# Performance work log

Measured on AMD Instinct MI355X. Metric: run time of the kernel, lower is better.

## Reference

```python
import jax, jax.numpy as jnp
import numpy as np

SOS = 1

def setup_inputs() -> dict:
    key = jax.random.key(0)
    ks = jax.random.split(key, 12)
    B, S, T, H, V = 64, 128, 32, 1024, 32000
    sc = 0.02
    return {
        'encoder_outputs': jax.random.normal(ks[0], (B, S, H), jnp.float32),
        'encoder_hidden': jax.random.normal(ks[1], (1, B, H), jnp.float32),
        'target_tensor': jax.random.randint(ks[2], (B, T), 0, V),
        'embedding': jax.random.normal(ks[3], (V, H), jnp.float32) * sc,
        'Wa': jax.random.normal(ks[4], (H, H), jnp.float32) * sc,
        'ba': jnp.zeros((H,), jnp.float32),
        'Ua': jax.random.normal(ks[5], (H, H), jnp.float32) * sc,
        'bu': jnp.zeros((H,), jnp.float32),
        'Va': jax.random.normal(ks[6], (1, H), jnp.float32) * sc,
        'bv': jnp.zeros((1,), jnp.float32),
        'W_ih': jax.random.normal(ks[7], (3 * H, 2 * H), jnp.float32) * sc,
        'b_ih': jnp.zeros((3 * H,), jnp.float32),
        'W_hh': jax.random.normal(ks[8], (3 * H, H), jnp.float32) * sc,
        'b_hh': jnp.zeros((3 * H,), jnp.float32),
        'W_out': jax.random.normal(ks[9], (V, H), jnp.float32) * sc,
        'b_out': jnp.zeros((V,), jnp.float32),
    }

def reference(encoder_outputs, encoder_hidden, target_tensor, embedding,
              Wa, ba, Ua, bu, Va, bv, W_ih, b_ih, W_hh, b_hh, W_out, b_out):
    B, S, H = encoder_outputs.shape
    T = target_tensor.shape[1]
    # teacher forcing: input at step i is SOS for i=0 else target[:, i-1]
    tokens = jnp.concatenate([jnp.full((B, 1), SOS, target_tensor.dtype),
                              target_tensor[:, :-1]], axis=1)  # (B,T)
    emb = embedding[tokens]  # (B,T,H); dropout is identity (eval)
    keys_proj = jnp.einsum('bsh,gh->bsg', encoder_outputs, Ua) + bu  # Ua(keys), (B,S,H)
    h0 = encoder_hidden[0]  # (B,H)

    def step(h, x_t):
        # Bahdanau attention: Va(tanh(Wa q + Ua k))
        q = h @ Wa.T + ba  # (B,H)
        scores = jnp.einsum('bsh,h->bs', jnp.tanh(q[:, None, :] + keys_proj), Va[0]) + bv[0]
        w = jax.nn.softmax(scores, axis=-1)  # (B,S)
        ctx = jnp.einsum('bs,bsh->bh', w, encoder_outputs)
        x = jnp.concatenate([x_t, ctx], axis=-1)  # (B,2H)
        # GRU cell (PyTorch convention)
        gi = x @ W_ih.T + b_ih
        gh = h @ W_hh.T + b_hh
        ir, iz, inn = jnp.split(gi, 3, axis=-1)
        hr, hz, hn = jnp.split(gh, 3, axis=-1)
        r = jax.nn.sigmoid(ir + hr)
        z = jax.nn.sigmoid(iz + hz)
        n = jnp.tanh(inn + r * hn)
        h_new = (1.0 - z) * n + z * h
        logits = h_new @ W_out.T + b_out  # (B,V)
        return h_new, (logits, w)

    h_final, (logits, weights) = jax.lax.scan(step, h0, jnp.swapaxes(emb, 0, 1))
    log_probs = jax.nn.log_softmax(jnp.swapaxes(logits, 0, 1), axis=-1)  # (B,T,V)
    attentions = jnp.swapaxes(weights, 0, 1)  # (B,T,S)
    return log_probs, h_final[None], attentions
```

## Files before the change

### kernel.cpp

```cpp
#include <hip/hip_runtime.h>


typedef unsigned short u16;
typedef __bf16 bf16x8 __attribute__((ext_vector_type(8)));
typedef float f32x4 __attribute__((ext_vector_type(4)));
typedef u16 u16x8 __attribute__((ext_vector_type(8)));

#define DEV __device__ __forceinline__

DEV u16 f2b(float f) {
  union { float f; unsigned u; } v; v.f = f;
  unsigned r = v.u + 0x7fffu + ((v.u >> 16) & 1u);
  return (u16)(r >> 16);
}
DEV float b2f(u16 b) {
  union { unsigned u; float f; } v; v.u = ((unsigned)b) << 16;
  return v.f;
}
DEV float sigm(float x) { return 1.f / (1.f + __expf(-x)); }
DEV float ftanh(float x) {
  x = fminf(fmaxf(x, -20.f), 20.f);
  float e = __expf(2.f * x);
  return (e - 1.f) / (e + 1.f);
}
DEV void gl16(const void* g, void* l) {
  __builtin_amdgcn_global_load_lds((const __attribute__((address_space(1))) void*)g,
                                   (__attribute__((address_space(3))) void*)l, 16, 0, 0);
}

__global__ __launch_bounds__(256) void prepk(const float* __restrict__ enc, const float* __restrict__ Ua,
                                             const float* __restrict__ Wa, const float* __restrict__ Whh,
                                             const float* __restrict__ Wout, const float* __restrict__ Wih,
                                             const float* __restrict__ embd, const int* __restrict__ tgt,
                                             const float* __restrict__ eh, u16* __restrict__ enc_b,
                                             u16* __restrict__ Ua_b, u16* __restrict__ Wa_b,
                                             u16* __restrict__ Whh_b, u16* __restrict__ Wout_b,
                                             u16* __restrict__ Wih1_b, u16* __restrict__ Wih2_b,
                                             u16* __restrict__ emb_b, float* __restrict__ hf,
                                             u16* __restrict__ hb0) {
  const long q0 = 2097152;
  const long q1 = q0 + 262144;
  const long q2 = q1 + 262144;
  const long q3 = q2 + 786432;
  const long q4 = q3 + 8192000;
  const long q5 = q4 + 1572864;
  const long q6 = q5 + 524288;
  const long q7 = q6 + 16384;
  long stride = (long)gridDim.x * 256;
  for (long i = (long)blockIdx.x * 256 + threadIdx.x; i < q7; i += stride) {
    if (i < q4) {
      const float* src; u16* dst; long off;
      if (i < q0) { src = enc; dst = enc_b; off = i; }
      else if (i < q1) { src = Ua; dst = Ua_b; off = i - q0; }
      else if (i < q2) { src = Wa; dst = Wa_b; off = i - q1; }
      else if (i < q3) { src = Whh; dst = Whh_b; off = i - q2; }
      else { src = Wout; dst = Wout_b; off = i - q3; }
      float4 v = ((const float4*)src)[off];
      ushort4 o; o.x = f2b(v.x); o.y = f2b(v.y); o.z = f2b(v.z); o.w = f2b(v.w);
      ((ushort4*)dst)[off] = o;
    } else if (i < q5) {
      long off = i - q4;
      long e = off * 4;
      int row = (int)(e >> 11), col = (int)(e & 2047);
      float4 v = ((const float4*)Wih)[off];
      ushort4 o; o.x = f2b(v.x); o.y = f2b(v.y); o.z = f2b(v.z); o.w = f2b(v.w);
      u16* dst = (col < 1024) ? (Wih1_b + (size_t)row * 1024 + col)
                              : (Wih2_b + (size_t)row * 1024 + col - 1024);
      *(ushort4*)dst = o;
    } else if (i < q6) {
      long off = i - q5;
      size_t e = (size_t)off * 4;
      int h = (int)(e & 1023);
      int bt = (int)(e >> 10);
      int b = bt >> 5, t = bt & 31;
      int tok = (t == 0) ? 1 : tgt[b * 32 + t - 1];
      const float* src = embd + (size_t)tok * 1024 + h;
      float4 v = *(const float4*)src;
      ushort4 o; o.x = f2b(v.x); o.y = f2b(v.y); o.z = f2b(v.z); o.w = f2b(v.w);
      *(ushort4*)(emb_b + e) = o;
    } else {
      long off = i - q6;
      float4 v = ((const float4*)eh)[off];
      ((float4*)hf)[off] = v;
      ushort4 o; o.x = f2b(v.x); o.y = f2b(v.y); o.z = f2b(v.z); o.w = f2b(v.w);
      ((ushort4*)hb0)[off] = o;
    }
  }
}

template <int MODE>
__global__ __launch_bounds__(256) void gemm_tile(const u16* __restrict__ A, const u16* __restrict__ Bm,
                                                 const float* __restrict__ bias, float* __restrict__ Cf,
                                                 u16* __restrict__ Cb, int K, int ldc, int nTM) {
  __shared__ __attribute__((aligned(16))) u16 As[128 * 32];
  __shared__ __attribute__((aligned(16))) u16 Bs[128 * 32];
  const int tid = threadIdx.x, lane = tid & 63, w = tid >> 6;
  const int chunk = gridDim.x >> 3, wg = blockIdx.x;
  const int id = (wg & 7) * chunk + (wg >> 3);
  const int m = id % nTM, n = id / nTM;
  const int m0 = m * 128, n0 = n * 128;
  const int wm = w >> 1, wn = w & 1;
  const int l16 = lane & 15, kg = lane >> 4;
  const int srow = lane >> 2;
  const int skk = (((lane & 3) ^ ((srow >> 1) & 3)) * 8);
  const int slot = (kg ^ ((l16 >> 1) & 3)) * 8;

  f32x4 acc[4][4];
#pragma unroll
  for (int i = 0; i < 4; ++i)
#pragma unroll
    for (int j = 0; j < 4; ++j) acc[i][j] = f32x4{0.f, 0.f, 0.f, 0.f};

  for (int k0 = 0; k0 < K; k0 += 32) {
#pragma unroll
    for (int ch = 0; ch < 2; ++ch) {
      int c = w + ch * 4;
      gl16(A + (size_t)(m0 + c * 16 + srow) * K + k0 + skk, &As[c * 512]);
      gl16(Bm + (size_t)(n0 + c * 16 + srow) * K + k0 + skk, &Bs[c * 512]);
    }
    __syncthreads();
    bf16x8 av[4], bv[4];
#pragma unroll
    for (int i = 0; i < 4; ++i) av[i] = *(const bf16x8*)&As[(wm * 4 + i) * 512 + l16 * 32 + slot];
#pragma unroll
    for (int j = 0; j < 4; ++j) bv[j] = *(const bf16x8*)&Bs[(wn * 4 + j) * 512 + l16 * 32 + slot];
#pragma unroll
    for (int i = 0; i < 4; ++i)
#pragma unroll
      for (int j = 0; j < 4; ++j)
        acc[i][j] = __builtin_amdgcn_mfma_f32_16x16x32_bf16(av[i], bv[j], acc[i][j], 0, 0, 0);
    __syncthreads();
  }
#pragma unroll
  for (int i = 0; i < 4; ++i) {
    int rowb = m0 + (wm * 4 + i) * 16 + kg * 4;
#pragma unroll
    for (int j = 0; j < 4; ++j) {
      int col = n0 + (wn * 4 + j) * 16 + l16;
      float bb = (MODE == 2) ? 0.f : bias[col];
#pragma unroll
      for (int r = 0; r < 4; ++r) {
        int row = rowb + r;
        float v = acc[i][j][r] + bb;
        if (MODE == 0) Cf[(size_t)row * ldc + col] = v;
        else Cb[(size_t)row * ldc + col] = f2b(v);
      }
    }
  }
}

template <int MODE, int MAP>
__global__ __launch_bounds__(256, 2) void gemm_wide(const u16* __restrict__ A, const u16* __restrict__ Bm,
                                                    const float* __restrict__ bias, float* __restrict__ Cf,
                                                    u16* __restrict__ Cb, int K, int ldc, int nTM) {
  __shared__ __attribute__((aligned(16))) u16 As[128 * 64];
  __shared__ __attribute__((aligned(16))) u16 Bs[256 * 64];
  const int tid = threadIdx.x, lane = tid & 63, w = tid >> 6;
  const int chunk = gridDim.x >> 3, wg = blockIdx.x;
  const int id = (wg & 7) * chunk + (wg >> 3);
  int m, n;
  if (MAP == 0) { int r_ = id % 80; m = r_ & 15; n = 5 * (id / 80) + (r_ >> 4); }
  else { m = id % nTM; n = id / nTM; }
  const int m0 = m * 128, n0 = n * 256;
  const int wm = w >> 1, wn = w & 1;
  const int l16 = lane & 15, kg = lane >> 4;
  const int srow = lane >> 2;
  const int skk = (((lane & 3) ^ ((srow >> 1) & 3)) * 8);
  const int slot = (kg ^ ((l16 >> 1) & 3)) * 8;

  f32x4 acc[4][8];
#pragma unroll
  for (int i = 0; i < 4; ++i)
#pragma unroll
    for (int j = 0; j < 8; ++j) acc[i][j] = f32x4{0.f, 0.f, 0.f, 0.f};

  for (int k0 = 0; k0 < K; k0 += 64) {
#pragma unroll
    for (int ch = 0; ch < 2; ++ch) {
      int c = w + ch * 4;
#pragma unroll
      for (int p = 0; p < 2; ++p)
        gl16(A + (size_t)(m0 + c * 16 + srow) * K + k0 + p * 32 + skk, &As[c * 1024 + p * 512]);
    }
#pragma unroll
    for (int ch = 0; ch < 4; ++ch) {
      int c = w + ch * 4;
#pragma unroll
      for (int p = 0; p < 2; ++p)
        gl16(Bm + (size_t)(n0 + c * 16 + srow) * K + k0 + p * 32 + skk, &Bs[c * 1024 + p * 512]);
    }
    __syncthreads();
#pragma unroll
    for (int p = 0; p < 2; ++p) {
      bf16x8 av[4], bv[8];
#pragma unroll
      for (int i = 0; i < 4; ++i)
        av[i] = *(const bf16x8*)&As[(wm * 4 + i) * 1024 + p * 512 + l16 * 32 + slot];
#pragma unroll
      for (int j = 0; j < 8; ++j)
        bv[j] = *(const bf16x8*)&Bs[(wn * 8 + j) * 1024 + p * 512 + l16 * 32 + slot];
#pragma unroll
      for (int i = 0; i < 4; ++i)
#pragma unroll
        for (int j = 0; j < 8; ++j)
          acc[i][j] = __builtin_amdgcn_mfma_f32_16x16x32_bf16(av[i], bv[j], acc[i][j], 0, 0, 0);
    }
    __syncthreads();
  }
#pragma unroll
  for (int i = 0; i < 4; ++i) {
    int rowb = m0 + (wm * 4 + i) * 16 + kg * 4;
#pragma unroll
    for (int j = 0; j < 8; ++j) {
      int col = n0 + (wn * 8 + j) * 16 + l16;
      float bb = (MODE == 2) ? 0.f : bias[col];
#pragma unroll
      for (int r = 0; r < 4; ++r) {
        int row = rowb + r;
        float v = acc[i][j][r] + bb;
        if (MODE == 2) {
          Cb[(size_t)row * ldc + col] = f2b(v);
        } else {
          int b_ = row & 63, t_ = row >> 6;
          size_t ro = ((size_t)b_ * 32 + t_) * ldc + col;
          if (MODE == 0) Cf[ro] = v; else Cb[ro] = f2b(v);
        }
      }
    }
  }
}

__global__ __launch_bounds__(256) void qkghk(const u16* __restrict__ hb, const u16* __restrict__ W1,
                                             float* __restrict__ qghp) {
  const int tid = threadIdx.x, lane = tid & 63, w = tid >> 6;
  const int l16 = lane & 15, kg = lane >> 4;
  const int pg = blockIdx.x >> 2, ks = blockIdx.x & 3;
  const u16* ap = hb + (size_t)(w * 16 + l16) * 1024 + ks * 256 + kg * 8;
  const u16* bp = W1 + (size_t)(pg * 16 + l16) * 1024 + ks * 256 + kg * 8;
  f32x4 a = {0.f, 0.f, 0.f, 0.f};
#pragma unroll
  for (int k0 = 0; k0 < 256; k0 += 32)
    a = __builtin_amdgcn_mfma_f32_16x16x32_bf16(*(const bf16x8*)(ap + k0), *(const bf16x8*)(bp + k0),
                                                a, 0, 0, 0);
  const int col = pg * 16 + l16;
#pragma unroll
  for (int r = 0; r < 4; ++r) {
    int b = w * 16 + kg * 4 + r;
    qghp[(size_t)ks * 262144 + b * 4096 + col] = a[r];
  }
}

__global__ __launch_bounds__(256) void scorekq(const float* __restrict__ qghp, const float* __restrict__ ba,
                                               const float* __restrict__ Va, const u16* __restrict__ kp,
                                               float* __restrict__ sc) {
  const int b = blockIdx.x >> 4, s16 = blockIdx.x & 15;
  const int tid = threadIdx.x, lane = tid & 63, w = tid >> 6;
  __shared__ float qs[1024], vas[1024];
#pragma unroll
  for (int j = 0; j < 4; ++j) {
    int e = tid + j * 256;
    qs[e] = qghp[b * 4096 + e] + qghp[262144 + b * 4096 + e] + qghp[524288 + b * 4096 + e] +
            qghp[786432 + b * 4096 + e] + ba[e];
    vas[e] = Va[e];
  }
  __syncthreads();
#pragma unroll
  for (int si = 0; si < 2; ++si) {
    int s = s16 * 8 + w * 2 + si;
    const bf16x8* kv = (const bf16x8*)(kp + ((size_t)b * 128 + s) * 1024);
    float a = 0.f;
#pragma unroll
    for (int i2 = 0; i2 < 2; ++i2) {
      int e = lane + 64 * i2;
      bf16x8 k8 = kv[e];
#pragma unroll
      for (int j = 0; j < 8; ++j) a += vas[e * 8 + j] * ftanh(qs[e * 8 + j] + (float)k8[j]);
    }
#pragma unroll
    for (int off = 32; off; off >>= 1) a += __shfl_xor(a, off);
    if (lane == 0) sc[b * 128 + s] = a;
  }
}

__global__ __launch_bounds__(512, 4) void wsumgate(const float* __restrict__ scb, const u16* __restrict__ encW2,
                                                   const float* __restrict__ gie, const float* __restrict__ qghp,
                                                   const float* __restrict__ bhh, float* __restrict__ hf,
                                                   u16* __restrict__ hbW, u16* __restrict__ hall,
                                                   float* __restrict__ hfin, float* __restrict__ att_out, int t) {
  const int b = blockIdx.x >> 3, ce = blockIdx.x & 7;
  const int tid = threadIdx.x, lane = tid & 63, w = tid >> 6;
  __shared__ float wsm[128];
  __shared__ float pa[32][3][128];
  if (w == 0) {
    float v0 = scb[b * 128 + lane], v1 = scb[b * 128 + 64 + lane];
    float mx = fmaxf(v0, v1);
#pragma unroll
    for (int off = 32; off; off >>= 1) mx = fmaxf(mx, __shfl_xor(mx, off));
    float e0 = __expf(v0 - mx), e1 = __expf(v1 - mx);
    float sm = e0 + e1;
#pragma unroll
    for (int off = 32; off; off >>= 1) sm += __shfl_xor(sm, off);
    float inv = 1.f / sm;
    e0 *= inv; e1 *= inv;
    wsm[lane] = e0; wsm[lane + 64] = e1;
    if (ce == 0) {
      size_t ao = ((size_t)b * 32 + t) * 128;
      att_out[ao + lane] = e0;
      att_out[ao + lane + 64] = e1;
    }
  }
  __syncthreads();
  const int cg8 = tid & 15, sg = tid >> 4;
  const int colBase = ce * 128 + cg8 * 8;
  float a0[8], a1[8], a2[8];
#pragma unroll
  for (int k = 0; k < 8; ++k) { a0[k] = 0.f; a1[k] = 0.f; a2[k] = 0.f; }
  const u16* ep = encW2 + ((size_t)b * 128 + sg * 4) * 3072 + colBase;
#pragma unroll
  for (int si = 0; si < 4; ++si) {
    float ws = wsm[sg * 4 + si];
    u16x8 v0 = *(const u16x8*)(ep);
    u16x8 v1 = *(const u16x8*)(ep + 1024);
    u16x8 v2 = *(const u16x8*)(ep + 2048);
#pragma unroll
    for (int k = 0; k < 8; ++k) {
      a0[k] += ws * b2f(v0[k]);
      a1[k] += ws * b2f(v1[k]);
      a2[k] += ws * b2f(v2[k]);
    }
    ep += 3072;
  }
  {
    f32x4 t0 = {a0[0], a0[1], a0[2], a0[3]}, t1 = {a0[4], a0[5], a0[6], a0[7]};
    *(f32x4*)&pa[sg][0][cg8 * 8] = t0; *(f32x4*)&pa[sg][0][cg8 * 8 + 4] = t1;
    f32x4 t2 = {a1[0], a1[1], a1[2], a1[3]}, t3 = {a1[4], a1[5], a1[6], a1[7]};
    *(f32x4*)&pa[sg][1][cg8 * 8] = t2; *(f32x4*)&pa[sg][1][cg8 * 8 + 4] = t3;
    f32x4 t4 = {a2[0], a2[1], a2[2], a2[3]}, t5 = {a2[4], a2[5], a2[6], a2[7]};
    *(f32x4*)&pa[sg][2][cg8 * 8] = t4; *(f32x4*)&pa[sg][2][cg8 * 8 + 4] = t5;
  }
  __syncthreads();
  if (tid < 128) {
    float g0 = 0.f, g1 = 0.f, g2 = 0.f;
#pragma unroll
    for (int s2 = 0; s2 < 32; ++s2) {
      g0 += pa[s2][0][tid]; g1 += pa[s2][1][tid]; g2 += pa[s2][2][tid];
    }
    const int c2 = ce * 128 + tid;
    const float* ge = gie + ((size_t)b * 32 + t) * 3072 + c2;
    const float* qg = qghp + (size_t)b * 4096 + 1024 + c2;
    float hr = qg[0] + qg[262144] + qg[524288] + qg[786432] + bhh[c2];
    float hz = qg[1024] + qg[1024 + 262144] + qg[1024 + 524288] + qg[1024 + 786432] + bhh[c2 + 1024];
    float hn = qg[2048] + qg[2048 + 262144] + qg[2048 + 524288] + qg[2048 + 786432] + bhh[c2 + 2048];
    float rr = sigm(g0 + ge[0] + hr);
    float zz = sigm(g1 + ge[1024] + hz);
    float nn = ftanh(g2 + ge[2048] + rr * hn);
    const int i = b * 1024 + c2;
    float hp = hf[i];
    float hv = (1.f - zz) * nn + zz * hp;
    hf[i] = hv;
    u16 h16 = f2b(hv);
    hbW[i] = h16;
    hall[((size_t)t * 64 + b) * 1024 + c2] = h16;
    if (t == 31) hfin[i] = hv;
  }
}

__global__ __launch_bounds__(256) void smaxctxk(const float* __restrict__ sc, const u16* __restrict__ encb,
                                                u16* __restrict__ ctxb, float* __restrict__ att_out, int t) {
  const int b = blockIdx.x >> 2, hq = blockIdx.x & 3;
  const int tid = threadIdx.x, lane = tid & 63, w = tid >> 6;
  __shared__ float wsm[128];
  if (w == 0) {
    float v0 = sc[b * 128 + lane], v1 = sc[b * 128 + 64 + lane];
    float mx = fmaxf(v0, v1);
#pragma unroll
    for (int off = 32; off; off >>= 1) mx = fmaxf(mx, __shfl_xor(mx, off));
    float e0 = __expf(v0 - mx), e1 = __expf(v1 - mx);
    float sm = e0 + e1;
#pragma unroll
    for (int off = 32; off; off >>= 1) sm += __shfl_xor(sm, off);
    float inv = 1.f / sm;
    e0 *= inv; e1 *= inv;
    wsm[lane] = e0; wsm[lane + 64] = e1;
    if (hq == 0) {
      size_t ao = ((size_t)b * 32 + t) * 128;
      att_out[ao + lane] = e0;
      att_out[ao + lane + 64] = e1;
    }
  }
  __syncthreads();
  const int h = hq * 256 + tid;
  const u16* ep = encb + (size_t)b * 131072 + h;
  float c = 0.f;
#pragma unroll 8
  for (int s = 0; s < 128; ++s) c += wsm[s] * b2f(ep[(size_t)s * 1024]);
  ctxb[(size_t)b * 1024 + h] = f2b(c);
}

__global__ __launch_bounds__(256) void gi2w(const u16* __restrict__ ctxb, const u16* __restrict__ Wih2,
                                            float* __restrict__ gic) {
  const int tid = threadIdx.x, lane = tid & 63, w = tid >> 6;
  const int l16 = lane & 15, kg = lane >> 4;
  const int c0 = blockIdx.x * 16;
  const u16* ap = ctxb + (size_t)(w * 16 + l16) * 1024 + kg * 8;
  const u16* bp = Wih2 + (size_t)(c0 + l16) * 1024 + kg * 8;
  f32x4 a0 = {0.f, 0.f, 0.f, 0.f}, a1 = {0.f, 0.f, 0.f, 0.f};
#pragma unroll 4
  for (int k0 = 0; k0 < 1024; k0 += 64) {
    a0 = __builtin_amdgcn_mfma_f32_16x16x32_bf16(*(const bf16x8*)(ap + k0), *(const bf16x8*)(bp + k0),
                                                 a0, 0, 0, 0);
    a1 = __builtin_amdgcn_mfma_f32_16x16x32_bf16(*(const bf16x8*)(ap + k0 + 32),
                                                 *(const bf16x8*)(bp + k0 + 32), a1, 0, 0, 0);
  }
  const int col = c0 + l16;
#pragma unroll
  for (int r = 0; r < 4; ++r) {
    int b = w * 16 + kg * 4 + r;
    gic[(size_t)b * 3072 + col] = a0[r] + a1[r];
  }
}

__global__ __launch_bounds__(256) void gatesq(const float* __restrict__ gic, const float* __restrict__ gie,
                                              const float* __restrict__ qghp, const float* __restrict__ bhh,
                                              float* __restrict__ hf, u16* __restrict__ hbW,
                                              u16* __restrict__ hall, float* __restrict__ hfin, int t) {
  const int i = blockIdx.x * 256 + threadIdx.x;
  const int b = i >> 10, col = i & 1023;
  const float* gi = gic + (size_t)b * 3072 + col;
  const float* ge = gie + ((size_t)b * 32 + t) * 3072 + col;
  const float* qg = qghp + (size_t)b * 4096 + 1024 + col;
  float hr = qg[0] + qg[262144] + qg[524288] + qg[786432] + bhh[col];
  float hz = qg[1024] + qg[1024 + 262144] + qg[1024 + 524288] + qg[1024 + 786432] + bhh[col + 1024];
  float hn = qg[2048] + qg[2048 + 262144] + qg[2048 + 524288] + qg[2048 + 786432] + bhh[col + 2048];
  float rr = sigm(gi[0] + ge[0] + hr);
  float zz = sigm(gi[1024] + ge[1024] + hz);
  float nn = ftanh(gi[2048] + ge[2048] + rr * hn);
  float hp = hf[i];
  float hv = (1.f - zz) * nn + zz * hp;
  hf[i] = hv;
  u16 h16 = f2b(hv);
  hbW[i] = h16;
  hall[((size_t)t * 64 + b) * 1024 + col] = h16;
  if (t == 31) hfin[i] = hv;
}

__global__ __launch_bounds__(256) void logsoftk(const u16* __restrict__ lg, float* __restrict__ out) {
  const int row = blockIdx.x, tid = threadIdx.x, lane = tid & 63, w = tid >> 6;
  const u16x8* p = (const u16x8*)(lg + (size_t)row * 32000);
  __shared__ float red[4];
  u16x8 d[16];
#pragma unroll
  for (int j = 0; j < 16; ++j) {
    int i = tid + j * 256;
    if (i < 4000) d[j] = p[i];
  }
  float mx = -3.0e38f;
#pragma unroll
  for (int j = 0; j < 16; ++j) {
    int i = tid + j * 256;
    if (i < 4000)
#pragma unroll
      for (int k = 0; k < 8; ++k) mx = fmaxf(mx, b2f(d[j][k]));
  }
#pragma unroll
  for (int off = 32; off; off >>= 1) mx = fmaxf(mx, __shfl_xor(mx, off));
  if (lane == 0) red[w] = mx;
  __syncthreads();
  mx = fmaxf(fmaxf(red[0], red[1]), fmaxf(red[2], red[3]));
  __syncthreads();
  float s = 0.f;
#pragma unroll
  for (int j = 0; j < 16; ++j) {
    int i = tid + j * 256;
    if (i < 4000)
#pragma unroll
      for (int k = 0; k < 8; ++k) s += __expf(b2f(d[j][k]) - mx);
  }
#pragma unroll
  for (int off = 32; off; off >>= 1) s += __shfl_xor(s, off);
  if (lane == 0) red[w] = s;
  __syncthreads();
  float c = mx + __logf(red[0] + red[1] + red[2] + red[3]);
  float* op = out + (size_t)row * 32000;
#pragma unroll
  for (int j = 0; j < 16; ++j) {
    int i = tid + j * 256;
    if (i < 4000) {
      f32x4 o0, o1;
#pragma unroll
      for (int k = 0; k < 4; ++k) { o0[k] = b2f(d[j][k]) - c; o1[k] = b2f(d[j][k + 4]) - c; }
      *(f32x4*)(op + i * 8) = o0;
      *(f32x4*)(op + i * 8 + 4) = o1;
    }
  }
}

__global__ __launch_bounds__(256) void rowstatk(const float* __restrict__ lp, float* __restrict__ c) {
  int row = blockIdx.x;
  const float4* p = (const float4*)(lp + (size_t)row * 32000);
  int tid = threadIdx.x, lane = tid & 63, w = tid >> 6;
  __shared__ float redm[4], reds[4];
  float mx = -3.0e38f;
  for (int i = tid; i < 8000; i += 256) {
    float4 v = p[i];
    mx = fmaxf(mx, fmaxf(fmaxf(v.x, v.y), fmaxf(v.z, v.w)));
  }
#pragma unroll
  for (int off = 32; off; off >>= 1) mx = fmaxf(mx, __shfl_xor(mx, off));
  if (lane == 0) redm[w] = mx;
  __syncthreads();
  mx = fmaxf(fmaxf(redm[0], redm[1]), fmaxf(redm[2], redm[3]));
  float s = 0.f;
  for (int i = tid; i < 8000; i += 256) {
    float4 v = p[i];
    s += __expf(v.x - mx) + __expf(v.y - mx) + __expf(v.z - mx) + __expf(v.w - mx);
  }
#pragma unroll
  for (int off = 32; off; off >>= 1) s += __shfl_xor(s, off);
  if (lane == 0) reds[w] = s;
  __syncthreads();
  if (tid == 0) c[row] = mx + __logf(reds[0] + reds[1] + reds[2] + reds[3]);
}

__global__ __launch_bounds__(256) void subk(float* __restrict__ lp, const float* __restrict__ c) {
  const long n4 = (long)64 * 32 * 32000 / 4;
  long stride = (long)gridDim.x * 256;
  for (long i = (long)blockIdx.x * 256 + threadIdx.x; i < n4; i += stride) {
    float4 v = ((float4*)lp)[i];
    float cc = c[i / 8000];
    v.x -= cc; v.y -= cc; v.z -= cc; v.w -= cc;
    ((float4*)lp)[i] = v;
  }
}

extern "C" void kernel_launch(void* const* d_in, const int* in_sizes, int n_in, void* d_out, int out_size,
                              void* d_ws, size_t ws_size, hipStream_t stream) {
  (void)in_sizes; (void)n_in; (void)out_size;
  constexpr int B = 64, S = 128, T = 32, H = 1024, V = 32000;

  const float* enc  = (const float*)d_in[0];
  const float* ehid = (const float*)d_in[1];
  const int*   tgt  = (const int*)d_in[2];
  const float* embd = (const float*)d_in[3];
  const float* Wa   = (const float*)d_in[4];
  const float* ba   = (const float*)d_in[5];
  const float* Ua   = (const float*)d_in[6];
  const float* bu   = (const float*)d_in[7];
  const float* Va   = (const float*)d_in[8];
  const float* Wih  = (const float*)d_in[10];
  const float* bih  = (const float*)d_in[11];
  const float* Whh  = (const float*)d_in[12];
  const float* bhh  = (const float*)d_in[13];
  const float* Wout = (const float*)d_in[14];
  const float* bout = (const float*)d_in[15];

  char* wp = (char*)d_ws;
  auto alloc = [&](size_t bytes) {
    char* p = wp;
    wp += (bytes + 255) & ~(size_t)255;
    return p;
  };
  u16* enc_b  = (u16*)alloc((size_t)B * S * H * 2);
  u16* kp_b   = (u16*)alloc((size_t)B * S * H * 2);
  u16* Ua_b   = (u16*)alloc((size_t)H * H * 2);
  u16* W1_b   = (u16*)alloc((size_t)4096 * 1024 * 2);
  u16* Wih1_b = (u16*)alloc((size_t)3072 * 1024 * 2);
  u16* Wih2_b = (u16*)alloc((size_t)3072 * 1024 * 2);
  u16* Wout_b = (u16*)alloc((size_t)V * H * 2);
  u16* emb_b  = (u16*)alloc((size_t)B * T * H * 2);
  u16* hall_b = (u16*)alloc((size_t)T * B * H * 2);
  float* gie  = (float*)alloc((size_t)B * T * 3072 * 4);
  float* qghp = (float*)alloc((size_t)4 * B * 4096 * 4);
  float* scb  = (float*)alloc((size_t)B * S * 4);
  float* gic  = (float*)alloc((size_t)B * 3072 * 4);
  u16* ctx_b  = (u16*)alloc((size_t)B * H * 2);
  u16* hb0    = (u16*)alloc((size_t)B * H * 2);
  u16* hb1    = (u16*)alloc((size_t)B * H * 2);
  float* h_f  = (float*)alloc((size_t)B * H * 4);
  float* rowc = (float*)alloc(2048 * 4);
  size_t base_need = (size_t)(wp - (char*)d_ws);
  u16* encW2 = (u16*)alloc((size_t)B * S * 3072 * 2);
  bool have_w2 = ((size_t)(wp - (char*)d_ws) <= ws_size);
  u16* lg_b = (u16*)alloc((size_t)B * T * V * 2);
  bool bflog = ((size_t)(wp - (char*)d_ws) <= ws_size);
  if (base_need > ws_size) return;

  float* out_lp = (float*)d_out;
  float* out_hf = out_lp + (size_t)B * T * V;
  float* out_at = out_hf + (size_t)B * H;

  u16* Wa_slot = W1_b;
  u16* Whh_slot = W1_b + (size_t)1024 * 1024;
  prepk<<<2048, 256, 0, stream>>>(enc, Ua, Wa, Whh, Wout, Wih, embd, tgt, ehid,
                                  enc_b, Ua_b, Wa_slot, Whh_slot, Wout_b,
                                  Wih1_b, Wih2_b, emb_b, h_f, hb0);

  gemm_tile<1><<<512, 256, 0, stream>>>(enc_b, Ua_b, bu, nullptr, kp_b, H, H, 64);
  gemm_tile<0><<<384, 256, 0, stream>>>(emb_b, Wih1_b, bih, gie, nullptr, H, 3072, 16);
  if (have_w2) {
    gemm_wide<2, 1><<<768, 256, 0, stream>>>(enc_b, Wih2_b, nullptr, nullptr, encW2, H, 3072, 64);
  }

  for (int t = 0; t < T; ++t) {
    u16* hbR = (t & 1) ? hb1 : hb0;
    u16* hbW = (t & 1) ? hb0 : hb1;
    qkghk<<<1024, 256, 0, stream>>>(hbR, W1_b, qghp);
    scorekq<<<1024, 256, 0, stream>>>(qghp, ba, Va, kp_b, scb);
    if (have_w2) {
      wsumgate<<<512, 512, 0, stream>>>(scb, encW2, gie, qghp, bhh, h_f, hbW, hall_b,
                                        out_hf, out_at, t);
    } else {
      smaxctxk<<<256, 256, 0, stream>>>(scb, enc_b, ctx_b, out_at, t);
      gi2w<<<192, 256, 0, stream>>>(ctx_b, Wih2_b, gic);
      gatesq<<<256, 256, 0, stream>>>(gic, gie, qghp, bhh, h_f, hbW, hall_b, out_hf, t);
    }
  }

  if (bflog) {
    gemm_wide<1, 0><<<2000, 256, 0, stream>>>(hall_b, Wout_b, bout, nullptr, lg_b, H, V, 16);
    logsoftk<<<2048, 256, 0, stream>>>(lg_b, out_lp);
  } else {
    gemm_wide<0, 0><<<2000, 256, 0, stream>>>(hall_b, Wout_b, bout, out_lp, nullptr, H, V, 16);
    rowstatk<<<2048, 256, 0, stream>>>(out_lp, rowc);
    subk<<<2048, 256, 0, stream>>>(out_lp, rowc);
  }
}
```

Before: 1.397 ms.

## Fuse query projection with attention score computation into one per-step kernel

Merges the per-step q/gh projection GEMM and the tanh score kernel into a single launch. 512 blocks each compute a 16-column slice of Wa·h over the full K and immediately apply tanh with the matching keys slice, writing partial scores per column group. The remaining 384 blocks compute W_hh·h with a 2-way K split. wsumgate then reduces the 64 partial score slices before the softmax. This removes one launch and the qghp round trip per timestep, at the cost of more partial-score traffic and a heavier reduction in wsumgate.

Measured after the change: 1.719 ms. 23.1% more time.

```diff
diff --git a/kernel.cpp b/kernel.cpp
--- a/kernel.cpp
+++ b/kernel.cpp
@@ -230,59 +230,63 @@
   }
 }
 
-__global__ __launch_bounds__(256) void qkghk(const u16* __restrict__ hb, const u16* __restrict__ W1,
-                                             float* __restrict__ qghp) {
+__global__ __launch_bounds__(256) void qkscork(const u16* __restrict__ hb, const u16* __restrict__ W1,
+                                               const float* __restrict__ ba, const float* __restrict__ Va,
+                                               const u16* __restrict__ kp, float* __restrict__ scp,
+                                               float* __restrict__ qghp) {
   const int tid = threadIdx.x, lane = tid & 63, w = tid >> 6;
   const int l16 = lane & 15, kg = lane >> 4;
-  const int pg = blockIdx.x >> 2, ks = blockIdx.x & 3;
-  const u16* ap = hb + (size_t)(w * 16 + l16) * 1024 + ks * 256 + kg * 8;
-  const u16* bp = W1 + (size_t)(pg * 16 + l16) * 1024 + ks * 256 + kg * 8;
-  f32x4 a = {0.f, 0.f, 0.f, 0.f};
-#pragma unroll
-  for (int k0 = 0; k0 < 256; k0 += 32)
-    a = __builtin_amdgcn_mfma_f32_16x16x32_bf16(*(const bf16x8*)(ap + k0), *(const bf16x8*)(bp + k0),
-                                                a, 0, 0, 0);
-  const int col = pg * 16 + l16;
-#pragma unroll
-  for (int r = 0; r < 4; ++r) {
-    int b = w * 16 + kg * 4 + r;
-    qghp[(size_t)ks * 262144 + b * 4096 + col] = a[r];
-  }
-}
-
-__global__ __launch_bounds__(256) void scorekq(const float* __restrict__ qghp, const float* __restrict__ ba,
-                                               const float* __restrict__ Va, const u16* __restrict__ kp,
-                                               float* __restrict__ sc) {
-  const int b = blockIdx.x >> 4, s16 = blockIdx.x & 15;
-  const int tid = threadIdx.x, lane = tid & 63, w = tid >> 6;
-  __shared__ float qs[1024], vas[1024];
-#pragma unroll
-  for (int j = 0; j < 4; ++j) {
-    int e = tid + j * 256;
-    qs[e] = qghp[b * 4096 + e] + qghp[262144 + b * 4096 + e] + qghp[524288 + b * 4096 + e] +
-            qghp[786432 + b * 4096 + e] + ba[e];
-    vas[e] = Va[e];
-  }
-  __syncthreads();
-#pragma unroll
-  for (int si = 0; si < 2; ++si) {
-    int s = s16 * 8 + w * 2 + si;
-    const bf16x8* kv = (const bf16x8*)(kp + ((size_t)b * 128 + s) * 1024);
-    float a = 0.f;
-#pragma unroll
-    for (int i2 = 0; i2 < 2; ++i2) {
-      int e = lane + 64 * i2;
-      bf16x8 k8 = kv[e];
-#pragma unroll
-      for (int j = 0; j < 8; ++j) a += vas[e * 8 + j] * ftanh(qs[e * 8 + j] + (float)k8[j]);
-    }
-#pragma unroll
-    for (int off = 32; off; off >>= 1) a += __shfl_xor(a, off);
-    if (lane == 0) sc[b * 128 + s] = a;
-  }
-}
-
-__global__ __launch_bounds__(512, 4) void wsumgate(const float* __restrict__ scb, const u16* __restrict__ encW2,
+  if (blockIdx.x < 512) {
+    const int hp = blockIdx.x >> 3, s8 = blockIdx.x & 7;
+    __shared__ float qs[64][17];
+    __shared__ float vas[16];
+    if (tid < 16) vas[tid] = Va[hp * 16 + tid];
+    const u16* ap = hb + (size_t)(w * 16 + l16) * 1024 + kg * 8;
+    const u16* bp = W1 + (size_t)(hp * 16 + l16) * 1024 + kg * 8;
+    f32x4 a = {0.f, 0.f, 0.f, 0.f};
+#pragma unroll
+    for (int k0 = 0; k0 < 1024; k0 += 32)
+      a = __builtin_amdgcn_mfma_f32_16x16x32_bf16(*(const bf16x8*)(ap + k0), *(const bf16x8*)(bp + k0),
+                                                  a, 0, 0, 0);
+    float bb = ba[hp * 16 + l16];
+#pragma unroll
+    for (int r = 0; r < 4; ++r) qs[w * 16 + kg * 4 + r][l16] = a[r] + bb;
+    __syncthreads();
+    const int b = tid & 63;
+#pragma unroll
+    for (int p = 0; p < 4; ++p) {
+      int sl = (tid >> 6) * 4 + p;
+      int s = s8 * 16 + sl;
+      const u16x8* kv = (const u16x8*)(kp + ((size_t)b * 128 + s) * 1024 + hp * 16);
+      u16x8 k0v = kv[0], k1v = kv[1];
+      float acc = 0.f;
+#pragma unroll
+      for (int j = 0; j < 8; ++j) acc += vas[j] * ftanh(qs[b][j] + b2f(k0v[j]));
+#pragma unroll
+      for (int j = 0; j < 8; ++j) acc += vas[8 + j] * ftanh(qs[b][8 + j] + b2f(k1v[j]));
+      scp[(size_t)hp * 8192 + b * 128 + s] = acc;
+    }
+  } else {
+    const int j2 = blockIdx.x - 512;
+    const int pg = j2 >> 1, ks = j2 & 1;
+    const u16* Whh = W1 + (size_t)1024 * 1024;
+    const u16* ap = hb + (size_t)(w * 16 + l16) * 1024 + ks * 512 + kg * 8;
+    const u16* bp = Whh + (size_t)(pg * 16 + l16) * 1024 + ks * 512 + kg * 8;
+    f32x4 a = {0.f, 0.f, 0.f, 0.f};
+#pragma unroll
+    for (int k0 = 0; k0 < 512; k0 += 32)
+      a = __builtin_amdgcn_mfma_f32_16x16x32_bf16(*(const bf16x8*)(ap + k0), *(const bf16x8*)(bp + k0),
+                                                  a, 0, 0, 0);
+    const int col = pg * 16 + l16;
+#pragma unroll
+    for (int r = 0; r < 4; ++r) {
+      int b = w * 16 + kg * 4 + r;
+      qghp[(size_t)ks * 196608 + b * 3072 + col] = a[r];
+    }
+  }
+}
+
+__global__ __launch_bounds__(512, 4) void wsumgate(const float* __restrict__ scp, const u16* __restrict__ encW2,
                                                    const float* __restrict__ gie, const float* __restrict__ qghp,
                                                    const float* __restrict__ bhh, float* __restrict__ hf,
                                                    u16* __restrict__ hbW, u16* __restrict__ hall,
@@ -290,9 +294,19 @@
   const int b = blockIdx.x >> 3, ce = blockIdx.x & 7;
   const int tid = threadIdx.x, lane = tid & 63, w = tid >> 6;
   __shared__ float wsm[128];
+  __shared__ float red4[4][128];
   __shared__ float pa[32][3][128];
+  {
+    const int s = tid & 127, q4 = tid >> 7;
+    float v = 0.f;
+#pragma unroll
+    for (int k = 0; k < 16; ++k) v += scp[(size_t)(q4 * 16 + k) * 8192 + b * 128 + s];
+    red4[q4][s] = v;
+  }
+  __syncthreads();
   if (w == 0) {
-    float v0 = scb[b * 128 + lane], v1 = scb[b * 128 + 64 + lane];
+    float v0 = red4[0][lane] + red4[1][lane] + red4[2][lane] + red4[3][lane];
+    float v1 = red4[0][lane + 64] + red4[1][lane + 64] + red4[2][lane + 64] + red4[3][lane + 64];
     float mx = fmaxf(v0, v1);
 #pragma unroll
     for (int off = 32; off; off >>= 1) mx = fmaxf(mx, __shfl_xor(mx, off));
@@ -347,10 +361,10 @@
     }
     const int c2 = ce * 128 + tid;
     const float* ge = gie + ((size_t)b * 32 + t) * 3072 + c2;
-    const float* qg = qghp + (size_t)b * 4096 + 1024 + c2;
-    float hr = qg[0] + qg[262144] + qg[524288] + qg[786432] + bhh[c2];
-    float hz = qg[1024] + qg[1024 + 262144] + qg[1024 + 524288] + qg[1024 + 786432] + bhh[c2 + 1024];
-    float hn = qg[2048] + qg[2048 + 262144] + qg[2048 + 524288] + qg[2048 + 786432] + bhh[c2 + 2048];
+    const float* qg = qghp + (size_t)b * 3072 + c2;
+    float hr = qg[0] + qg[196608] + bhh[c2];
+    float hz = qg[1024] + qg[1024 + 196608] + bhh[c2 + 1024];
+    float hn = qg[2048] + qg[2048 + 196608] + bhh[c2 + 2048];
     float rr = sigm(g0 + ge[0] + hr);
     float zz = sigm(g1 + ge[1024] + hz);
     float nn = ftanh(g2 + ge[2048] + rr * hn);
@@ -362,6 +376,58 @@
     hbW[i] = h16;
     hall[((size_t)t * 64 + b) * 1024 + c2] = h16;
     if (t == 31) hfin[i] = hv;
+  }
+}
+
+__global__ __launch_bounds__(256) void qkghk(const u16* __restrict__ hb, const u16* __restrict__ W1,
+                                             float* __restrict__ qghp) {
+  const int tid = threadIdx.x, lane = tid & 63, w = tid >> 6;
+  const int l16 = lane & 15, kg = lane >> 4;
+  const int pg = blockIdx.x >> 2, ks = blockIdx.x & 3;
+  const u16* ap = hb + (size_t)(w * 16 + l16) * 1024 + ks * 256 + kg * 8;
+  const u16* bp = W1 + (size_t)(pg * 16 + l16) * 1024 + ks * 256 + kg * 8;
+  f32x4 a = {0.f, 0.f, 0.f, 0.f};
+#pragma unroll
+  for (int k0 = 0; k0 < 256; k0 += 32)
+    a = __builtin_amdgcn_mfma_f32_16x16x32_bf16(*(const bf16x8*)(ap + k0), *(const bf16x8*)(bp + k0),
+                                                a, 0, 0, 0);
+  const int col = pg * 16 + l16;
+#pragma unroll
+  for (int r = 0; r < 4; ++r) {
+    int b = w * 16 + kg * 4 + r;
+    qghp[(size_t)ks * 262144 + b * 4096 + col] = a[r];
+  }
+}
+
+__global__ __launch_bounds__(256) void scorekq(const float* __restrict__ qghp, const float* __restrict__ ba,
+                                               const float* __restrict__ Va, const u16* __restrict__ kp,
+                                               float* __restrict__ sc) {
+  const int b = blockIdx.x >> 4, s16 = blockIdx.x & 15;
+  const int tid = threadIdx.x, lane = tid & 63, w = tid >> 6;
+  __shared__ float qs[1024], vas[1024];
+#pragma unroll
+  for (int j = 0; j < 4; ++j) {
+    int e = tid + j * 256;
+    qs[e] = qghp[b * 4096 + e] + qghp[262144 + b * 4096 + e] + qghp[524288 + b * 4096 + e] +
+            qghp[786432 + b * 4096 + e] + ba[e];
+    vas[e] = Va[e];
+  }
+  __syncthreads();
+#pragma unroll
+  for (int si = 0; si < 2; ++si) {
+    int s = s16 * 8 + w * 2 + si;
+    const bf16x8* kv = (const bf16x8*)(kp + ((size_t)b * 128 + s) * 1024);
+    float a = 0.f;
+#pragma unroll
+    for (int i2 = 0; i2 < 2; ++i2) {
+      int e = lane + 64 * i2;
+      bf16x8 k8 = kv[e];
+#pragma unroll
+      for (int j = 0; j < 8; ++j) a += vas[e * 8 + j] * ftanh(qs[e * 8 + j] + (float)k8[j]);
+    }
+#pragma unroll
+    for (int off = 32; off; off >>= 1) a += __shfl_xor(a, off);
+    if (lane == 0) sc[b * 128 + s] = a;
   }
 }
 
@@ -571,6 +637,7 @@
   u16* hall_b = (u16*)alloc((size_t)T * B * H * 2);
   float* gie  = (float*)alloc((size_t)B * T * 3072 * 4);
   float* qghp = (float*)alloc((size_t)4 * B * 4096 * 4);
+  float* scp  = (float*)alloc((size_t)64 * B * S * 4);
   float* scb  = (float*)alloc((size_t)B * S * 4);
   float* gic  = (float*)alloc((size_t)B * 3072 * 4);
   u16* ctx_b  = (u16*)alloc((size_t)B * H * 2);
@@ -604,12 +671,13 @@
   for (int t = 0; t < T; ++t) {
     u16* hbR = (t & 1) ? hb1 : hb0;
     u16* hbW = (t & 1) ? hb0 : hb1;
-    qkghk<<<1024, 256, 0, stream>>>(hbR, W1_b, qghp);
-    scorekq<<<1024, 256, 0, stream>>>(qghp, ba, Va, kp_b, scb);
     if (have_w2) {
-      wsumgate<<<512, 512, 0, stream>>>(scb, encW2, gie, qghp, bhh, h_f, hbW, hall_b,
+      qkscork<<<896, 256, 0, stream>>>(hbR, W1_b, ba, Va, kp_b, scp, qghp);
+      wsumgate<<<512, 512, 0, stream>>>(scp, encW2, gie, qghp, bhh, h_f, hbW, hall_b,
                                         out_hf, out_at, t);
     } else {
+      qkghk<<<1024, 256, 0, stream>>>(hbR, W1_b, qghp);
+      scorekq<<<1024, 256, 0, stream>>>(qghp, ba, Va, kp_b, scb);
       smaxctxk<<<256, 256, 0, stream>>>(scb, enc_b, ctx_b, out_at, t);
       gi2w<<<192, 256, 0, stream>>>(ctx_b, Wih2_b, gic);
       gatesq<<<256, 256, 0, stream>>>(gic, gie, qghp, bhh, h_f, hbW, hall_b, out_hf, t);
```
